# Optimization experiments

Hardware: AMD Instinct MI355X
Metric: run time of the kernel (lower is better)

The kernel has to match this reference:

```python
import jax, jax.numpy as jnp
import numpy as np

R = 8  # rnn_radius
C = 64  # channels


def _shift(x, dh, dw):
    # out[b, h, w, c] = x[b, h - dh, w - dw, c], zero padded (matches SAME conv with a single masked tap)
    B, H, W, Cc = x.shape
    x = jnp.pad(x, ((0, 0), (max(dh, 0), max(-dh, 0)), (max(dw, 0), max(-dw, 0)), (0, 0)))
    return x[:, max(-dh, 0):max(-dh, 0) + H, max(-dw, 0):max(-dw, 0) + W, :]


def _direction(x, W, dh, dw):
    # recurrent: t = relu(shift(t) @ W); acc = x + sum_t over R steps
    def step(carry, _):
        t, acc = carry
        t = jax.nn.relu(jnp.einsum('bhwc,cd->bhwd', _shift(t, dh, dw), W))
        return (t, acc + t), None
    (_, acc), _ = jax.lax.scan(step, (x, x), None, length=R)
    return acc


def setup_inputs() -> dict:
    key = jax.random.key(0)
    kx, kl, kr, ku, kd = jax.random.split(key, 5)
    x = jax.random.normal(kx, (8, 192, 192, C), dtype=jnp.float32)
    # masked kernels reduce to a single CxC channel-mix matrix per direction
    # (keras 'random_normal' initializer: stddev 0.05)
    W_left = jax.random.normal(kl, (C, C), dtype=jnp.float32) * 0.05
    W_right = jax.random.normal(kr, (C, C), dtype=jnp.float32) * 0.05
    W_up = jax.random.normal(ku, (C, C), dtype=jnp.float32) * 0.05
    W_down = jax.random.normal(kd, (C, C), dtype=jnp.float32) * 0.05
    return {"x": x, "W_left": W_left, "W_right": W_right, "W_up": W_up, "W_down": W_down}


def reference(x, W_left, W_right, W_up, W_down):
    # kernel_switch tap positions: left -> out[w]=in[w-1]; right -> out[w]=in[w+1];
    # up -> out[h]=in[h-1]; down -> out[h]=in[h+1]
    outs = [
        _direction(x, W_left, 0, 1),
        _direction(x, W_right, 0, -1),
        _direction(x, W_up, 1, 0),
        _direction(x, W_down, -1, 0),
    ]
    return jnp.concatenate(outs, axis=3)
```

## Files before the change

kernel.cpp:

```cpp
#include <hip/hip_runtime.h>
#include <hip/hip_bf16.h>


#define HD 192
#define CH 64
#define RSTEPS 8
#define TSTRIDE 72
#define SLOTS 193

typedef __attribute__((ext_vector_type(8))) short short8v;
typedef __attribute__((ext_vector_type(4))) float float4v;

static __device__ __forceinline__ short f2bf_rne(float f) {
    unsigned u = __float_as_uint(f);
    u += 0x7FFFu + ((u >> 16) & 1u);
    return (short)(u >> 16);
}

__global__ __launch_bounds__(256, 4) void spatial_rnn_kernel(
    const float* __restrict__ x,
    const float* __restrict__ Wl,
    const float* __restrict__ Wr,
    const float* __restrict__ Wu,
    const float* __restrict__ Wd,
    float* __restrict__ out)
{
    __shared__ __align__(16) short tb[SLOTS * TSTRIDE];

    const int tid  = threadIdx.x;
    const int dir  = blockIdx.y;
    const int line = blockIdx.x;
    const int b    = line / HD;
    const int rc   = line - b * HD;

    const float* Wp = (dir == 0) ? Wl : (dir == 1) ? Wr : (dir == 2) ? Wu : Wd;

    int xbase, xstride, obase, ostride;
    if (dir == 0) {
        xbase   = (b * HD + rc) * HD * CH;
        xstride = CH;
        obase   = (b * HD + rc) * HD * 256;
        ostride = 256;
    } else if (dir == 1) {
        xbase   = ((b * HD + rc) * HD + (HD - 1)) * CH;
        xstride = -CH;
        obase   = ((b * HD + rc) * HD + (HD - 1)) * 256 + 64;
        ostride = -256;
    } else if (dir == 2) {
        xbase   = b * HD * HD * CH + rc * CH;
        xstride = HD * CH;
        obase   = b * HD * HD * 256 + rc * 256 + 128;
        ostride = HD * 256;
    } else {
        xbase   = ((b * HD + (HD - 1)) * HD + rc) * CH;
        xstride = -HD * CH;
        obase   = ((b * HD + (HD - 1)) * HD + rc) * 256 + 192;
        ostride = -HD * 256;
    }

    const int lane = tid & 63;
    const int wv   = tid >> 6;
    const int q4   = lane >> 4;
    const int l16  = lane & 15;

    if (tid < TSTRIDE) tb[tid] = 0;

    float4v acc[3][4];
    #pragma unroll
    for (int i = 0; i < 3; ++i) {
        const int p = (wv + i * 4) * 16 + l16;
        #pragma unroll
        for (int dt = 0; dt < 4; ++dt) {
            const float4 v = *(const float4*)(x + xbase + p * xstride + dt * 16 + q4 * 4);
            acc[i][dt] = (float4v){v.x, v.y, v.z, v.w};
            __hip_bfloat162 h01 = __float22bfloat162_rn(make_float2(v.x, v.y));
            __hip_bfloat162 h23 = __float22bfloat162_rn(make_float2(v.z, v.w));
            uint2 wpk;
            __builtin_memcpy(&wpk.x, &h01, 4);
            __builtin_memcpy(&wpk.y, &h23, 4);
            *(uint2*)(tb + (p + 1) * TSTRIDE + dt * 16 + q4 * 4) = wpk;
        }
    }

    short8v Af[2][4];
    #pragma unroll
    for (int kc = 0; kc < 2; ++kc)
        #pragma unroll
        for (int dt = 0; dt < 4; ++dt)
            #pragma unroll
            for (int j = 0; j < 8; ++j)
                Af[kc][dt][j] = f2bf_rne(Wp[(kc * 32 + q4 * 8 + j) * CH + dt * 16 + l16]);

    __syncthreads();

    for (int k = 0; k < RSTEPS; ++k) {
        short8v B0[3], B1[3];
        #pragma unroll
        for (int i = 0; i < 3; ++i) {
            const int slot = (wv + i * 4) * 16 + l16;
            B0[i] = *(const short8v*)(tb + slot * TSTRIDE + q4 * 8);
            B1[i] = *(const short8v*)(tb + slot * TSTRIDE + 32 + q4 * 8);
        }
        __syncthreads();
        #pragma unroll
        for (int i = 0; i < 3; ++i) {
            const int pb = (wv + i * 4) * 16;
            #pragma unroll
            for (int dt = 0; dt < 4; ++dt) {
                float4v d = {0.f, 0.f, 0.f, 0.f};
                d = __builtin_amdgcn_mfma_f32_16x16x32_bf16(Af[0][dt], B0[i], d, 0, 0, 0);
                d = __builtin_amdgcn_mfma_f32_16x16x32_bf16(Af[1][dt], B1[i], d, 0, 0, 0);
                float v0 = fmaxf(d[0], 0.f);
                float v1 = fmaxf(d[1], 0.f);
                float v2 = fmaxf(d[2], 0.f);
                float v3 = fmaxf(d[3], 0.f);
                acc[i][dt][0] += v0; acc[i][dt][1] += v1;
                acc[i][dt][2] += v2; acc[i][dt][3] += v3;
                if (k < RSTEPS - 1) {
                    __hip_bfloat162 h01 = __float22bfloat162_rn(make_float2(v0, v1));
                    __hip_bfloat162 h23 = __float22bfloat162_rn(make_float2(v2, v3));
                    uint2 wpk;
                    __builtin_memcpy(&wpk.x, &h01, 4);
                    __builtin_memcpy(&wpk.y, &h23, 4);
                    *(uint2*)(tb + (pb + l16 + 1) * TSTRIDE + dt * 16 + q4 * 4) = wpk;
                }
            }
        }
        if (k < RSTEPS - 1) __syncthreads();
    }

    #pragma unroll
    for (int i = 0; i < 3; ++i) {
        const int p = (wv + i * 4) * 16 + l16;
        #pragma unroll
        for (int dt = 0; dt < 4; ++dt) {
            float4 o;
            o.x = acc[i][dt][0]; o.y = acc[i][dt][1];
            o.z = acc[i][dt][2]; o.w = acc[i][dt][3];
            *(float4*)(out + obase + p * ostride + dt * 16 + q4 * 4) = o;
        }
    }
}

extern "C" void kernel_launch(void* const* d_in, const int* in_sizes, int n_in,
                              void* d_out, int out_size, void* d_ws, size_t ws_size,
                              hipStream_t stream) {
    const float* x  = (const float*)d_in[0];
    const float* Wl = (const float*)d_in[1];
    const float* Wr = (const float*)d_in[2];
    const float* Wu = (const float*)d_in[3];
    const float* Wd = (const float*)d_in[4];
    float* outp = (float*)d_out;
    dim3 grid(8 * HD, 4);
    spatial_rnn_kernel<<<grid, 256, 0, stream>>>(x, Wl, Wr, Wu, Wd, outp);
}
```

Before: 417.6 us.

## Swizzle LDS layout, double-buffer wave boundary rows, drop mid-step barrier

Rows in shared memory lose their padding (stride 72 becomes 64) and use an XOR swizzle to avoid bank conflicts. Each wave now owns a contiguous band of positions. The state crossing between waves goes through a small ping-pong boundary buffer, which removes the barrier between the reads and writes of each step. The grid is flattened so that consecutive blocks cover different batches and directions, and launch bounds ask for 6 blocks per CU. The cost is more complex indexing, and correctness now depends on the parity-based boundary buffering.

New measurement: 1.202 ms. +187.8%, slower.

```diff
diff --git a/kernel.cpp b/kernel.cpp
--- a/kernel.cpp
+++ b/kernel.cpp
@@ -5,8 +5,9 @@
 #define HD 192
 #define CH 64
 #define RSTEPS 8
-#define TSTRIDE 72
-#define SLOTS 193
+#define TS 64
+#define SLOTS 192
+#define BND (SLOTS * TS)
 
 typedef __attribute__((ext_vector_type(8))) short short8v;
 typedef __attribute__((ext_vector_type(4))) float float4v;
@@ -17,7 +18,7 @@
     return (short)(u >> 16);
 }
 
-__global__ __launch_bounds__(256, 4) void spatial_rnn_kernel(
+__global__ __launch_bounds__(256, 6) void spatial_rnn_kernel(
     const float* __restrict__ x,
     const float* __restrict__ Wl,
     const float* __restrict__ Wr,
@@ -25,13 +26,14 @@
     const float* __restrict__ Wd,
     float* __restrict__ out)
 {
-    __shared__ __align__(16) short tb[SLOTS * TSTRIDE];
+    __shared__ __align__(16) short tb[SLOTS * TS + 8 * TS];
 
-    const int tid  = threadIdx.x;
-    const int dir  = blockIdx.y;
-    const int line = blockIdx.x;
-    const int b    = line / HD;
-    const int rc   = line - b * HD;
+    const int tid = threadIdx.x;
+    const int bid = blockIdx.x;
+    const int b   = bid & 7;
+    const int idx = bid >> 3;
+    const int dir = idx & 3;
+    const int rc  = idx >> 2;
 
     const float* Wp = (dir == 0) ? Wl : (dir == 1) ? Wr : (dir == 2) ? Wu : Wd;
 
@@ -63,12 +65,15 @@
     const int q4   = lane >> 4;
     const int l16  = lane & 15;
 
-    if (tid < TSTRIDE) tb[tid] = 0;
+    if (tid < 32) ((int*)tb)[tid] = 0;
 
     float4v acc[3][4];
     #pragma unroll
     for (int i = 0; i < 3; ++i) {
-        const int p = (wv + i * 4) * 16 + l16;
+        const int p   = (3 * wv + i) * 16 + l16;
+        const int wsz = (l16 + 1) & 7;
+        int wbase = (p + 1) * TS;
+        if (i == 2 && l16 == 15) wbase = BND + (4 + wv) * TS;
         #pragma unroll
         for (int dt = 0; dt < 4; ++dt) {
             const float4 v = *(const float4*)(x + xbase + p * xstride + dt * 16 + q4 * 4);
@@ -78,7 +83,7 @@
             uint2 wpk;
             __builtin_memcpy(&wpk.x, &h01, 4);
             __builtin_memcpy(&wpk.y, &h23, 4);
-            *(uint2*)(tb + (p + 1) * TSTRIDE + dt * 16 + q4 * 4) = wpk;
+            *(uint2*)(tb + wbase + (((2 * dt + (q4 >> 1)) ^ wsz) << 3) + ((q4 & 1) << 2)) = wpk;
         }
     }
 
@@ -95,16 +100,21 @@
 
     for (int k = 0; k < RSTEPS; ++k) {
         short8v B0[3], B1[3];
+        const int prb = ((k & 1) ^ 1) << 2;
         #pragma unroll
         for (int i = 0; i < 3; ++i) {
-            const int slot = (wv + i * 4) * 16 + l16;
-            B0[i] = *(const short8v*)(tb + slot * TSTRIDE + q4 * 8);
-            B1[i] = *(const short8v*)(tb + slot * TSTRIDE + 32 + q4 * 8);
+            const int slot = (3 * wv + i) * 16 + l16;
+            const int sz   = l16 & 7;
+            int base = slot * TS;
+            if (i == 0 && l16 == 0 && wv > 0) base = BND + (prb + wv - 1) * TS;
+            B0[i] = *(const short8v*)(tb + base + ((q4 ^ sz) << 3));
+            B1[i] = *(const short8v*)(tb + base + (((q4 + 4) ^ sz) << 3));
         }
-        __syncthreads();
         #pragma unroll
         for (int i = 0; i < 3; ++i) {
-            const int pb = (wv + i * 4) * 16;
+            const int wsz = (l16 + 1) & 7;
+            int wbase = ((3 * wv + i) * 16 + l16 + 1) * TS;
+            if (i == 2 && l16 == 15) wbase = BND + (((k & 1) << 2) + wv) * TS;
             #pragma unroll
             for (int dt = 0; dt < 4; ++dt) {
                 float4v d = {0.f, 0.f, 0.f, 0.f};
@@ -122,7 +132,7 @@
                     uint2 wpk;
                     __builtin_memcpy(&wpk.x, &h01, 4);
                     __builtin_memcpy(&wpk.y, &h23, 4);
-                    *(uint2*)(tb + (pb + l16 + 1) * TSTRIDE + dt * 16 + q4 * 4) = wpk;
+                    *(uint2*)(tb + wbase + (((2 * dt + (q4 >> 1)) ^ wsz) << 3) + ((q4 & 1) << 2)) = wpk;
                 }
             }
         }
@@ -131,7 +141,7 @@
 
     #pragma unroll
     for (int i = 0; i < 3; ++i) {
-        const int p = (wv + i * 4) * 16 + l16;
+        const int p = (3 * wv + i) * 16 + l16;
         #pragma unroll
         for (int dt = 0; dt < 4; ++dt) {
             float4 o;
@@ -151,6 +161,6 @@
     const float* Wu = (const float*)d_in[3];
     const float* Wd = (const float*)d_in[4];
     float* outp = (float*)d_out;
-    dim3 grid(8 * HD, 4);
+    dim3 grid(8 * HD * 4);
     spatial_rnn_kernel<<<grid, 256, 0, stream>>>(x, Wl, Wr, Wu, Wd, outp);
 }
```
